# Kernel tuning notes

Measured on AMD Instinct MI355X. Metric: run time of the kernel, lower is better.

The kernel has to match this reference:

```python
import jax, jax.numpy as jnp
import numpy as np

MIN_NORM = 1e-15
PROJ_EPS = 4e-3  # PoincareBall.proj eps for float32
C = 1.0          # curvature


def _artanh(x):
    return jnp.arctanh(jnp.clip(x, -1 + 1e-7, 1 - 1e-7))


def _mobius_add(x, y, c):
    x2 = jnp.sum(x * x, -1, keepdims=True)
    y2 = jnp.sum(y * y, -1, keepdims=True)
    xy = jnp.sum(x * y, -1, keepdims=True)
    num = (1 + 2 * c * xy + c * y2) * x + (1 - c * x2) * y
    denom = 1 + 2 * c * xy + c * c * x2 * y2
    return num / jnp.maximum(denom, MIN_NORM)


def _sqdist(p1, p2, c):
    sqrt_c = c ** 0.5
    ma = _mobius_add(-p1, p2, c)
    dist = _artanh(sqrt_c * jnp.linalg.norm(ma, axis=-1)) * 2.0 / sqrt_c
    return dist ** 2


def _logmap0(p, c):
    sqrt_c = c ** 0.5
    p_norm = jnp.maximum(jnp.linalg.norm(p, axis=-1, keepdims=True), MIN_NORM)
    return p / p_norm / sqrt_c * _artanh(sqrt_c * p_norm)


def _expmap0(u, c):
    sqrt_c = c ** 0.5
    u_norm = jnp.maximum(jnp.linalg.norm(u, axis=-1, keepdims=True), MIN_NORM)
    return jnp.tanh(sqrt_c * u_norm) * u / (sqrt_c * u_norm)


def _proj(x, c):
    norm = jnp.maximum(jnp.linalg.norm(x, axis=-1, keepdims=True), MIN_NORM)
    maxnorm = (1 - PROJ_EPS) / (c ** 0.5)
    return jnp.where(norm > maxnorm, x / norm * maxnorm, x)


def setup_inputs() -> dict:
    key = jax.random.key(0)
    k1, k2 = jax.random.split(key)
    N, D, E = 100000, 64, 1600000
    # points on the Poincare ball (small norms, then projected)
    x = _proj(0.01 * jax.random.normal(k1, (N, D), dtype=jnp.float32), C)
    edge_index = jax.random.randint(k2, (2, E), 0, N, dtype=jnp.int64)
    beta = jnp.full((1,), 1e-2, dtype=jnp.float32)  # HypAggAtt.beta param
    con = jnp.zeros((1,), dtype=jnp.float32)        # HypAggAtt.con param
    return {"x": x, "beta": beta, "con": con, "edge_index": edge_index}


def reference(x, beta, con, edge_index):
    c = C
    N = x.shape[0]
    row, col = edge_index[0], edge_index[1]
    # per-edge hyperbolic attention logits: exp(-beta * sqdist + con)
    dist = _sqdist(x[row], x[col], c)            # [E]
    edge_e = jnp.exp(-beta[0] * dist + con[0])   # [E]
    x_t = _logmap0(x, c)                         # [N, D] tangent features
    # SpecialSpmm: sparse(row,col,edge_e) @ x_t  -> scatter-add over rows
    support = jax.ops.segment_sum(edge_e[:, None] * x_t[col], row, num_segments=N)
    e_rowsum = jax.ops.segment_sum(edge_e, row, num_segments=N) + 1e-10
    support = support / e_rowsum[:, None]
    return _proj(_expmap0(support, c), c)
```

## Files before the change

kernel.cpp:

```cpp
#include <hip/hip_runtime.h>
#include <math.h>

#define D 64
#define MIN_NORM 1e-15f
#define PROJ_MAXNORM 0.996f
#define RPB 64
#define BINCAP 1280
#define MAXBIN 2048
#define EPB 4096
#define BT 512

typedef __attribute__((ext_vector_type(8))) short short8;
typedef __attribute__((ext_vector_type(4))) float float4_;

__device__ __forceinline__ float wave_reduce_sum(float v) {
#pragma unroll
    for (int m = 1; m < 64; m <<= 1)
        v += __shfl_xor(v, m, 64);
    return v;
}

__device__ __forceinline__ float fast_artanh(float z) {
    z = fminf(z, 1.0f - 1e-7f);
    return 0.5f * __logf((1.0f + z) * __builtin_amdgcn_rcpf(1.0f - z));
}

__device__ __forceinline__ unsigned short f2bf(float x) {
    unsigned int b = __float_as_uint(x);
    return (unsigned short)((b + 0x7fffu + ((b >> 16) & 1u)) >> 16);
}

__device__ __forceinline__ float bf2f(unsigned short u) {
    return __uint_as_float(((unsigned int)u) << 16);
}

__global__ void bin_kernel(const float* __restrict__ x,
                           unsigned short* __restrict__ x_bf,
                           float2* __restrict__ snf,
                           const int* __restrict__ row_idx,
                           const int* __restrict__ col_idx,
                           int* __restrict__ cursor,
                           unsigned int* __restrict__ binData,
                           int E, int N, int nbins, int edgeBlocks) {
    __shared__ int hist[MAXBIN];
    __shared__ int base[MAXBIN];
    if ((int)blockIdx.x < edgeBlocks) {
        int e0 = blockIdx.x * EPB;
        int e1 = min(E, e0 + EPB);
        for (int i = threadIdx.x; i < nbins; i += BT) hist[i] = 0;
        __syncthreads();
        if (e1 - e0 == EPB) {
#pragma unroll
            for (int it = 0; it < EPB / (BT * 4); ++it) {
                int4 r = *(const int4*)(row_idx + e0 + it * (BT * 4) + (int)threadIdx.x * 4);
                atomicAdd(&hist[r.x >> 6], 1);
                atomicAdd(&hist[r.y >> 6], 1);
                atomicAdd(&hist[r.z >> 6], 1);
                atomicAdd(&hist[r.w >> 6], 1);
            }
        } else {
            for (int e = e0 + (int)threadIdx.x; e < e1; e += BT)
                atomicAdd(&hist[row_idx[e] >> 6], 1);
        }
        __syncthreads();
        for (int i = threadIdx.x; i < nbins; i += BT) {
            int h = hist[i];
            base[i] = h ? atomicAdd(&cursor[i], h) : 0;
        }
        __syncthreads();
        if (e1 - e0 == EPB) {
#pragma unroll
            for (int it = 0; it < EPB / (BT * 4); ++it) {
                int o = e0 + it * (BT * 4) + (int)threadIdx.x * 4;
                int4 r = *(const int4*)(row_idx + o);
                int4 c = *(const int4*)(col_idx + o);
                int b0 = r.x >> 6, b1 = r.y >> 6, b2 = r.z >> 6, b3 = r.w >> 6;
                int k0 = atomicAdd(&base[b0], 1);
                int k1 = atomicAdd(&base[b1], 1);
                int k2 = atomicAdd(&base[b2], 1);
                int k3 = atomicAdd(&base[b3], 1);
                if (k0 < BINCAP) binData[(size_t)b0 * BINCAP + k0] = ((unsigned int)(r.x & 63) << 17) | (unsigned int)c.x;
                if (k1 < BINCAP) binData[(size_t)b1 * BINCAP + k1] = ((unsigned int)(r.y & 63) << 17) | (unsigned int)c.y;
                if (k2 < BINCAP) binData[(size_t)b2 * BINCAP + k2] = ((unsigned int)(r.z & 63) << 17) | (unsigned int)c.z;
                if (k3 < BINCAP) binData[(size_t)b3 * BINCAP + k3] = ((unsigned int)(r.w & 63) << 17) | (unsigned int)c.w;
            }
        } else {
            for (int e = e0 + (int)threadIdx.x; e < e1; e += BT) {
                int r = row_idx[e];
                int c = col_idx[e];
                int b = r >> 6;
                int rk = atomicAdd(&base[b], 1);
                if (rk < BINCAP)
                    binData[(size_t)b * BINCAP + rk] =
                        ((unsigned int)(r & 63) << 17) | (unsigned int)c;
            }
        }
    } else {
        int nb = blockIdx.x - edgeBlocks;
        int node = nb * (BT / 16) + ((int)threadIdx.x >> 4);
        int j = threadIdx.x & 15;
        if (node >= N) return;
        float4 v = *((const float4*)(x + (size_t)node * D) + j);
        float s = v.x * v.x + v.y * v.y + v.z * v.z + v.w * v.w;
#pragma unroll
        for (int m = 1; m < 16; m <<= 1)
            s += __shfl_xor(s, m, 64);
        float pn = fmaxf(sqrtf(s), MIN_NORM);
        float f = fast_artanh(pn) / pn;
        ushort4 o;
        o.x = f2bf(v.x); o.y = f2bf(v.y); o.z = f2bf(v.z); o.w = f2bf(v.w);
        *((ushort4*)(x_bf + (size_t)node * D) + j) = o;
        if (j == 0) snf[node] = make_float2(s, f);
    }
}

__global__ void fused_kernel(const unsigned short* __restrict__ x_bf,
                             const float2* __restrict__ snf,
                             const unsigned int* __restrict__ binData,
                             const int* __restrict__ cursor,
                             const float* __restrict__ beta,
                             const float* __restrict__ con,
                             float* __restrict__ out, int N) {
    __shared__ int cnt[RPB];
    __shared__ int off[RPB];
    __shared__ int cur[RPB];
    __shared__ int colsm[BINCAP];

    int b = blockIdx.x;
    int len = min(cursor[b], BINCAP);
    const unsigned int* bd = binData + (size_t)b * BINCAP;

    if (threadIdx.x < RPB) { cnt[threadIdx.x] = 0; cur[threadIdx.x] = 0; }
    __syncthreads();
    for (int i = threadIdx.x; i < len; i += BT)
        atomicAdd(&cnt[bd[i] >> 17], 1);
    __syncthreads();
    if (threadIdx.x < 64) {
        int v = cnt[threadIdx.x], inc = v;
#pragma unroll
        for (int m = 1; m < 64; m <<= 1) {
            int t = __shfl_up(inc, m, 64);
            if ((int)threadIdx.x >= m) inc += t;
        }
        off[threadIdx.x] = inc - v;
    }
    __syncthreads();
    for (int i = threadIdx.x; i < len; i += BT) {
        unsigned int p = bd[i];
        int rl = p >> 17;
        int rk = atomicAdd(&cur[rl], 1);
        colsm[off[rl] + rk] = (int)(p & 0x1FFFFu);
    }
    __syncthreads();

    int wid = threadIdx.x >> 6;
    int lane = threadIdx.x & 63;
    int jj = lane & 15;
    int qd = lane >> 4;
    int src = ((jj >> 2) << 4) | jj;
    float B = beta[0], C0 = con[0];
    float4_ zero4 = {0.0f, 0.0f, 0.0f, 0.0f};

    for (int rl = wid; rl < RPB; rl += 8) {
        int row = b * RPB + rl;
        if (row >= N) break;
        int rlen = cnt[rl];
        int start = off[rl];
        int end = start + rlen;

        const unsigned short* xr = x_bf + (size_t)row * D + qd * 8;
        short8 bfr0 = *(const short8*)xr;
        short8 bfr1 = *(const short8*)(xr + 32);
        float x2 = snf[row].x;

        float acc[16];
#pragma unroll
        for (int i = 0; i < 16; i++) acc[i] = 0.0f;
        float wacc = 0.0f;

        for (int j0 = start; j0 < end; j0 += 16) {
            int idx = j0 + jj;
            bool valid = idx < end;
            int cw = colsm[valid ? idx : end - 1];
            const unsigned short* rp = x_bf + (size_t)cw * D + qd * 8;
            short8 af0 = *(const short8*)rp;
            short8 af1 = *(const short8*)(rp + 32);
            float2 sf = snf[cw];

            float4_ d4 = __builtin_amdgcn_mfma_f32_16x16x32_bf16(af0, bfr0, zero4, 0, 0, 0);
            d4 = __builtin_amdgcn_mfma_f32_16x16x32_bf16(af1, bfr1, d4, 0, 0, 0);

            float sel01 = (jj & 1) ? d4[1] : d4[0];
            float sel23 = (jj & 1) ? d4[3] : d4[2];
            float dsel  = (jj & 2) ? sel23 : sel01;
            float d = __shfl(dsel, src, 64);

            float y2 = sf.x;
            float a_ = 1.0f - 2.0f * d + y2;
            float b_ = 1.0f - x2;
            float num2 = a_ * a_ * x2 - 2.0f * a_ * b_ * d + b_ * b_ * y2;
            float den = fmaxf(1.0f - 2.0f * d + x2 * y2, MIN_NORM);
            float man = sqrtf(fmaxf(num2, 0.0f)) * __builtin_amdgcn_rcpf(den);
            float at = fast_artanh(man);
            float w = __expf(-B * 4.0f * at * at + C0);
            w = valid ? w : 0.0f;
            float wf = w * sf.y;
            wacc += w;
#pragma unroll
            for (int j = 0; j < 8; j++) {
                acc[j]     += wf * bf2f((unsigned short)af0[j]);
                acc[8 + j] += wf * bf2f((unsigned short)af1[j]);
            }
        }

#pragma unroll
        for (int m = 1; m < 16; m <<= 1)
            wacc += __shfl_xor(wacc, m, 64);

#pragma unroll
        for (int k = 0; k < 4; k++) {
            bool hi = (lane >> k) & 1;
            int half = 8 >> k;
#pragma unroll
            for (int i = 0; i < half; i++) {
                float a = acc[2 * i], bb = acc[2 * i + 1];
                float keep = hi ? bb : a;
                float send = hi ? a : bb;
                acc[i] = keep + __shfl_xor(send, 1 << k, 64);
            }
        }
        int f = qd * 8 + (jj & 7) + 32 * (jj >> 3);

        float s = acc[0] * __builtin_amdgcn_rcpf(wacc + 1e-10f);
        float n2 = wave_reduce_sum(s * s);
        float sq = sqrtf(n2);
        float un = fmaxf(sq, MIN_NORM);
        float e2 = __expf(2.0f * un);
        float th = (e2 - 1.0f) * __builtin_amdgcn_rcpf(e2 + 1.0f);
        float tt = th * __builtin_amdgcn_rcpf(un);
        float o = tt * s;
        float on = th * sq * __builtin_amdgcn_rcpf(un);
        if (on > PROJ_MAXNORM)
            o = o / fmaxf(on, MIN_NORM) * PROJ_MAXNORM;
        out[row * D + f] = o;
    }
}

extern "C" void kernel_launch(void* const* d_in, const int* in_sizes, int n_in,
                              void* d_out, int out_size, void* d_ws, size_t ws_size,
                              hipStream_t stream) {
    const float* x    = (const float*)d_in[0];
    const float* beta = (const float*)d_in[1];
    const float* con  = (const float*)d_in[2];
    const int*   ei   = (const int*)d_in[3];

    int N = in_sizes[0] / D;
    int E = in_sizes[3] / 2;
    const int* row_idx = ei;
    const int* col_idx = ei + E;
    float* out = (float*)d_out;

    int nbins = (N + RPB - 1) / RPB;

    float2*         snf     = (float2*)d_ws;
    unsigned short* x_bf    = (unsigned short*)(snf + N);
    unsigned int*   binData = (unsigned int*)(x_bf + (size_t)N * D);
    int*            cursor  = (int*)(binData + (size_t)nbins * BINCAP);

    hipMemsetAsync(cursor, 0, (size_t)nbins * sizeof(int), stream);

    int edgeBlocks = (E + EPB - 1) / EPB;
    int nodeBlocks = (N + (BT / 16) - 1) / (BT / 16);

    bin_kernel<<<edgeBlocks + nodeBlocks, BT, 0, stream>>>(
        x, x_bf, snf, row_idx, col_idx, cursor, binData, E, N, nbins, edgeBlocks);

    fused_kernel<<<nbins, BT, 0, stream>>>(x_bf, snf, binData, cursor,
                                           beta, con, out, N);
}
```

Baseline: 174.9 us.

## Map one row per lane group so each wave processes sixteen rows at once

The fused kernel now assigns each of the 16 column-lanes in a wave to a different destination row. Each wave loops edge slots up to the maximum degree among its 16 rows, instead of looping over one row's edges 16 at a time. This removes the per-row butterfly reduction of the accumulators and the full-wave norm reduction, and writes the output with float4 stores. The bin size doubles to 128 rows per block, with a two-segment prefix scan. In exchange, lanes whose rows have lower degree sit idle while the wave runs to the group's maximum degree. Rows past N in the last block also read x_bf and snf beyond their end.

New measurement: 176.3 us. About the same (+0.8%).

```diff
diff --git a/kernel.cpp b/kernel.cpp
--- a/kernel.cpp
+++ b/kernel.cpp
@@ -4,21 +4,14 @@
 #define D 64
 #define MIN_NORM 1e-15f
 #define PROJ_MAXNORM 0.996f
-#define RPB 64
-#define BINCAP 1280
-#define MAXBIN 2048
+#define RPB 128
+#define BINCAP 2560
+#define MAXBIN 1024
 #define EPB 4096
 #define BT 512
 
 typedef __attribute__((ext_vector_type(8))) short short8;
 typedef __attribute__((ext_vector_type(4))) float float4_;
-
-__device__ __forceinline__ float wave_reduce_sum(float v) {
-#pragma unroll
-    for (int m = 1; m < 64; m <<= 1)
-        v += __shfl_xor(v, m, 64);
-    return v;
-}
 
 __device__ __forceinline__ float fast_artanh(float z) {
     z = fminf(z, 1.0f - 1e-7f);
@@ -53,14 +46,14 @@
 #pragma unroll
             for (int it = 0; it < EPB / (BT * 4); ++it) {
                 int4 r = *(const int4*)(row_idx + e0 + it * (BT * 4) + (int)threadIdx.x * 4);
-                atomicAdd(&hist[r.x >> 6], 1);
-                atomicAdd(&hist[r.y >> 6], 1);
-                atomicAdd(&hist[r.z >> 6], 1);
-                atomicAdd(&hist[r.w >> 6], 1);
+                atomicAdd(&hist[r.x >> 7], 1);
+                atomicAdd(&hist[r.y >> 7], 1);
+                atomicAdd(&hist[r.z >> 7], 1);
+                atomicAdd(&hist[r.w >> 7], 1);
             }
         } else {
             for (int e = e0 + (int)threadIdx.x; e < e1; e += BT)
-                atomicAdd(&hist[row_idx[e] >> 6], 1);
+                atomicAdd(&hist[row_idx[e] >> 7], 1);
         }
         __syncthreads();
         for (int i = threadIdx.x; i < nbins; i += BT) {
@@ -74,25 +67,25 @@
                 int o = e0 + it * (BT * 4) + (int)threadIdx.x * 4;
                 int4 r = *(const int4*)(row_idx + o);
                 int4 c = *(const int4*)(col_idx + o);
-                int b0 = r.x >> 6, b1 = r.y >> 6, b2 = r.z >> 6, b3 = r.w >> 6;
+                int b0 = r.x >> 7, b1 = r.y >> 7, b2 = r.z >> 7, b3 = r.w >> 7;
                 int k0 = atomicAdd(&base[b0], 1);
                 int k1 = atomicAdd(&base[b1], 1);
                 int k2 = atomicAdd(&base[b2], 1);
                 int k3 = atomicAdd(&base[b3], 1);
-                if (k0 < BINCAP) binData[(size_t)b0 * BINCAP + k0] = ((unsigned int)(r.x & 63) << 17) | (unsigned int)c.x;
-                if (k1 < BINCAP) binData[(size_t)b1 * BINCAP + k1] = ((unsigned int)(r.y & 63) << 17) | (unsigned int)c.y;
-                if (k2 < BINCAP) binData[(size_t)b2 * BINCAP + k2] = ((unsigned int)(r.z & 63) << 17) | (unsigned int)c.z;
-                if (k3 < BINCAP) binData[(size_t)b3 * BINCAP + k3] = ((unsigned int)(r.w & 63) << 17) | (unsigned int)c.w;
+                if (k0 < BINCAP) binData[(size_t)b0 * BINCAP + k0] = ((unsigned int)(r.x & 127) << 17) | (unsigned int)c.x;
+                if (k1 < BINCAP) binData[(size_t)b1 * BINCAP + k1] = ((unsigned int)(r.y & 127) << 17) | (unsigned int)c.y;
+                if (k2 < BINCAP) binData[(size_t)b2 * BINCAP + k2] = ((unsigned int)(r.z & 127) << 17) | (unsigned int)c.z;
+                if (k3 < BINCAP) binData[(size_t)b3 * BINCAP + k3] = ((unsigned int)(r.w & 127) << 17) | (unsigned int)c.w;
             }
         } else {
             for (int e = e0 + (int)threadIdx.x; e < e1; e += BT) {
                 int r = row_idx[e];
                 int c = col_idx[e];
-                int b = r >> 6;
+                int b = r >> 7;
                 int rk = atomicAdd(&base[b], 1);
                 if (rk < BINCAP)
                     binData[(size_t)b * BINCAP + rk] =
-                        ((unsigned int)(r & 63) << 17) | (unsigned int)c;
+                        ((unsigned int)(r & 127) << 17) | (unsigned int)c;
             }
         }
     } else {
@@ -124,6 +117,7 @@
     __shared__ int cnt[RPB];
     __shared__ int off[RPB];
     __shared__ int cur[RPB];
+    __shared__ int tot[2];
     __shared__ int colsm[BINCAP];
 
     int b = blockIdx.x;
@@ -131,19 +125,23 @@
     const unsigned int* bd = binData + (size_t)b * BINCAP;
 
     if (threadIdx.x < RPB) { cnt[threadIdx.x] = 0; cur[threadIdx.x] = 0; }
+    if (threadIdx.x == 0) colsm[0] = 0;
     __syncthreads();
     for (int i = threadIdx.x; i < len; i += BT)
         atomicAdd(&cnt[bd[i] >> 17], 1);
     __syncthreads();
-    if (threadIdx.x < 64) {
+    if (threadIdx.x < RPB) {
         int v = cnt[threadIdx.x], inc = v;
 #pragma unroll
         for (int m = 1; m < 64; m <<= 1) {
             int t = __shfl_up(inc, m, 64);
-            if ((int)threadIdx.x >= m) inc += t;
+            if (((int)threadIdx.x & 63) >= m) inc += t;
         }
         off[threadIdx.x] = inc - v;
-    }
+        if (((int)threadIdx.x & 63) == 63) tot[threadIdx.x >> 6] = inc;
+    }
+    __syncthreads();
+    if (threadIdx.x >= 64 && threadIdx.x < RPB) off[threadIdx.x] += tot[0];
     __syncthreads();
     for (int i = threadIdx.x; i < len; i += BT) {
         unsigned int p = bd[i];
@@ -158,91 +156,95 @@
     int jj = lane & 15;
     int qd = lane >> 4;
     int src = ((jj >> 2) << 4) | jj;
-    float B = beta[0], C0 = con[0];
+    float Bc = beta[0], C0 = con[0];
     float4_ zero4 = {0.0f, 0.0f, 0.0f, 0.0f};
 
-    for (int rl = wid; rl < RPB; rl += 8) {
-        int row = b * RPB + rl;
-        if (row >= N) break;
-        int rlen = cnt[rl];
-        int start = off[rl];
-        int end = start + rlen;
-
-        const unsigned short* xr = x_bf + (size_t)row * D + qd * 8;
-        short8 bfr0 = *(const short8*)xr;
-        short8 bfr1 = *(const short8*)(xr + 32);
-        float x2 = snf[row].x;
-
-        float acc[16];
-#pragma unroll
-        for (int i = 0; i < 16; i++) acc[i] = 0.0f;
-        float wacc = 0.0f;
-
-        for (int j0 = start; j0 < end; j0 += 16) {
-            int idx = j0 + jj;
-            bool valid = idx < end;
-            int cw = colsm[valid ? idx : end - 1];
-            const unsigned short* rp = x_bf + (size_t)cw * D + qd * 8;
-            short8 af0 = *(const short8*)rp;
-            short8 af1 = *(const short8*)(rp + 32);
-            float2 sf = snf[cw];
-
-            float4_ d4 = __builtin_amdgcn_mfma_f32_16x16x32_bf16(af0, bfr0, zero4, 0, 0, 0);
-            d4 = __builtin_amdgcn_mfma_f32_16x16x32_bf16(af1, bfr1, d4, 0, 0, 0);
-
-            float sel01 = (jj & 1) ? d4[1] : d4[0];
-            float sel23 = (jj & 1) ? d4[3] : d4[2];
-            float dsel  = (jj & 2) ? sel23 : sel01;
-            float d = __shfl(dsel, src, 64);
-
-            float y2 = sf.x;
-            float a_ = 1.0f - 2.0f * d + y2;
-            float b_ = 1.0f - x2;
-            float num2 = a_ * a_ * x2 - 2.0f * a_ * b_ * d + b_ * b_ * y2;
-            float den = fmaxf(1.0f - 2.0f * d + x2 * y2, MIN_NORM);
-            float man = sqrtf(fmaxf(num2, 0.0f)) * __builtin_amdgcn_rcpf(den);
-            float at = fast_artanh(man);
-            float w = __expf(-B * 4.0f * at * at + C0);
-            w = valid ? w : 0.0f;
-            float wf = w * sf.y;
-            wacc += w;
-#pragma unroll
-            for (int j = 0; j < 8; j++) {
-                acc[j]     += wf * bf2f((unsigned short)af0[j]);
-                acc[8 + j] += wf * bf2f((unsigned short)af1[j]);
-            }
-        }
-
-#pragma unroll
-        for (int m = 1; m < 16; m <<= 1)
-            wacc += __shfl_xor(wacc, m, 64);
-
-#pragma unroll
-        for (int k = 0; k < 4; k++) {
-            bool hi = (lane >> k) & 1;
-            int half = 8 >> k;
-#pragma unroll
-            for (int i = 0; i < half; i++) {
-                float a = acc[2 * i], bb = acc[2 * i + 1];
-                float keep = hi ? bb : a;
-                float send = hi ? a : bb;
-                acc[i] = keep + __shfl_xor(send, 1 << k, 64);
-            }
-        }
-        int f = qd * 8 + (jj & 7) + 32 * (jj >> 3);
-
-        float s = acc[0] * __builtin_amdgcn_rcpf(wacc + 1e-10f);
-        float n2 = wave_reduce_sum(s * s);
-        float sq = sqrtf(n2);
-        float un = fmaxf(sq, MIN_NORM);
-        float e2 = __expf(2.0f * un);
-        float th = (e2 - 1.0f) * __builtin_amdgcn_rcpf(e2 + 1.0f);
-        float tt = th * __builtin_amdgcn_rcpf(un);
-        float o = tt * s;
-        float on = th * sq * __builtin_amdgcn_rcpf(un);
-        if (on > PROJ_MAXNORM)
-            o = o / fmaxf(on, MIN_NORM) * PROJ_MAXNORM;
-        out[row * D + f] = o;
+    int rl = wid * 16 + jj;
+    int row = b * RPB + rl;
+    int rlen = cnt[rl];
+    int start = off[rl];
+    int safe = rlen > 0 ? start + rlen - 1 : 0;
+
+    int ml = rlen;
+#pragma unroll
+    for (int m = 1; m < 16; m <<= 1)
+        ml = max(ml, __shfl_xor(ml, m, 64));
+
+    const unsigned short* xr = x_bf + (size_t)row * D + qd * 8;
+    short8 bfr0 = *(const short8*)xr;
+    short8 bfr1 = *(const short8*)(xr + 32);
+    float x2 = snf[row].x;
+
+    float acc[16];
+#pragma unroll
+    for (int i = 0; i < 16; i++) acc[i] = 0.0f;
+    float wacc = 0.0f;
+
+    for (int t = 0; t < ml; ++t) {
+        bool valid = t < rlen;
+        int cw = colsm[valid ? start + t : safe];
+        const unsigned short* rp = x_bf + (size_t)cw * D + qd * 8;
+        short8 af0 = *(const short8*)rp;
+        short8 af1 = *(const short8*)(rp + 32);
+        float2 sf = snf[cw];
+
+        float4_ d4 = __builtin_amdgcn_mfma_f32_16x16x32_bf16(af0, bfr0, zero4, 0, 0, 0);
+        d4 = __builtin_amdgcn_mfma_f32_16x16x32_bf16(af1, bfr1, d4, 0, 0, 0);
+
+        float sel01 = (jj & 1) ? d4[1] : d4[0];
+        float sel23 = (jj & 1) ? d4[3] : d4[2];
+        float dsel  = (jj & 2) ? sel23 : sel01;
+        float d = __shfl(dsel, src, 64);
+
+        float y2 = sf.x;
+        float a_ = 1.0f - 2.0f * d + y2;
+        float b_ = 1.0f - x2;
+        float num2 = a_ * a_ * x2 - 2.0f * a_ * b_ * d + b_ * b_ * y2;
+        float den = fmaxf(1.0f - 2.0f * d + x2 * y2, MIN_NORM);
+        float man = sqrtf(fmaxf(num2, 0.0f)) * __builtin_amdgcn_rcpf(den);
+        float at = fast_artanh(man);
+        float w = __expf(-Bc * 4.0f * at * at + C0);
+        w = valid ? w : 0.0f;
+        float wf = w * sf.y;
+        wacc += w;
+#pragma unroll
+        for (int j = 0; j < 8; j++) {
+            acc[j]     += wf * bf2f((unsigned short)af0[j]);
+            acc[8 + j] += wf * bf2f((unsigned short)af1[j]);
+        }
+    }
+
+    float inv = __builtin_amdgcn_rcpf(wacc + 1e-10f);
+    float s[16];
+    float loc = 0.0f;
+#pragma unroll
+    for (int j = 0; j < 16; j++) {
+        s[j] = acc[j] * inv;
+        loc += s[j] * s[j];
+    }
+    loc += __shfl_xor(loc, 16, 64);
+    loc += __shfl_xor(loc, 32, 64);
+    float n2 = loc;
+    float sq = sqrtf(n2);
+    float un = fmaxf(sq, MIN_NORM);
+    float e2 = __expf(2.0f * un);
+    float th = (e2 - 1.0f) * __builtin_amdgcn_rcpf(e2 + 1.0f);
+    float tt = th * __builtin_amdgcn_rcpf(un);
+    float on = th * sq * __builtin_amdgcn_rcpf(un);
+    float scale = tt;
+    if (on > PROJ_MAXNORM)
+        scale = tt / fmaxf(on, MIN_NORM) * PROJ_MAXNORM;
+
+    if (row < N) {
+        float* op = out + (size_t)row * D;
+        float4 v0 = make_float4(scale * s[0],  scale * s[1],  scale * s[2],  scale * s[3]);
+        float4 v1 = make_float4(scale * s[4],  scale * s[5],  scale * s[6],  scale * s[7]);
+        float4 v2 = make_float4(scale * s[8],  scale * s[9],  scale * s[10], scale * s[11]);
+        float4 v3 = make_float4(scale * s[12], scale * s[13], scale * s[14], scale * s[15]);
+        *(float4*)(op + qd * 8)          = v0;
+        *(float4*)(op + qd * 8 + 4)      = v1;
+        *(float4*)(op + 32 + qd * 8)     = v2;
+        *(float4*)(op + 32 + qd * 8 + 4) = v3;
     }
 }
 
```
